# Optimization experiments

Hardware: AMD Instinct MI355X
Metric: run time of the kernel (lower is better)

## Reference

```python
import jax, jax.numpy as jnp
import numpy as np

TOP_K = 8
NUM_EXPERTS = 64
TEMPERATURE = 1.0
ALPHA = 0.01
EPS = 1e-20


def setup_inputs() -> dict:
    key = jax.random.key(0)
    k1, k2 = jax.random.split(key)
    hidden_states = jax.random.normal(k1, (4, 8192, 1024), dtype=jnp.float32)
    # kaiming_uniform-ish scale for the router weight
    bound = 1.0 / np.sqrt(1024.0)
    weight = jax.random.uniform(k2, (NUM_EXPERTS, 1024), dtype=jnp.float32,
                                minval=-bound, maxval=bound)
    return {"hidden_states": hidden_states, "weight": weight}


def reference(hidden_states, weight):
    bsz, seq_len, hidden_dim = hidden_states.shape
    flat = hidden_states.reshape(-1, hidden_dim)            # [N, H], N = bsz*seq_len
    logits = jnp.einsum('nh,eh->ne', flat, weight) / TEMPERATURE  # [N, E]
    scores = jax.nn.softmax(logits, axis=-1)                # [N, E]
    topk_weight, topk_idx = jax.lax.top_k(scores, TOP_K)    # [N, k] each
    # renormalize top-k probabilities
    topk_weight = topk_weight / (topk_weight.sum(axis=-1, keepdims=True) + EPS)
    # aux load-balancing loss (seq_aux=False branch), scores detached
    scores_aux = jax.lax.stop_gradient(scores)
    idx_flat = topk_idx.reshape(-1)                         # [N*k]
    ce = jnp.zeros((NUM_EXPERTS,), dtype=jnp.float32).at[idx_flat].add(1.0)
    ce = ce / idx_flat.shape[0]                             # mean of one-hot rows
    pi = scores_aux.mean(axis=0)                            # [E]
    fi = ce * NUM_EXPERTS
    aux_loss = (pi * fi).sum() * ALPHA
    return topk_idx, topk_weight, aux_loss
```

## Files before the change

### kernel.cpp

```cpp
#include <hip/hip_runtime.h>

#define H 1024
#define E 64
#define BT 64
#define THETA 1e-4f

typedef __attribute__((ext_vector_type(4))) float f4;
typedef __attribute__((ext_vector_type(2))) float f2;

__device__ __forceinline__ void pkfma(f2& acc, f2 a, f2 b) {
    asm("v_pk_fma_f32 %0, %1, %2, %0" : "+v"(acc) : "v"(a), "v"(b));
}

__device__ __forceinline__ void async16(const void* g, void* l) {
    __builtin_amdgcn_global_load_lds(
        (const __attribute__((address_space(1))) unsigned int*)g,
        (__attribute__((address_space(3))) unsigned int*)l,
        16, 0, 0);
}

__global__ __launch_bounds__(256, 2)
void gate_main(const float* __restrict__ hs, const float* __restrict__ wt,
               float* __restrict__ out, float* __restrict__ pi_ws,
               float* __restrict__ ce_ws, unsigned int* __restrict__ risk_cnt,
               unsigned int* __restrict__ risk_list, unsigned int risk_cap,
               int n_tokens) {
    __shared__ float smem[16384];
    const int t = threadIdx.x;
    const int wave = t >> 6, lane = t & 63;
    const int tok_base = blockIdx.x * BT;
    const int tg = t >> 4;
    const int eg = t & 15;

    f2 acc[4][4];
    #pragma unroll
    for (int j = 0; j < 4; ++j)
        #pragma unroll
        for (int i = 0; i < 4; ++i) acc[j][i] = (f2){0.f, 0.f};

    auto stage = [&](int c, int b) {
        const int bb = b * 8192;
        #pragma unroll
        for (int q = 0; q < 4; ++q) {
            const int L = q * 256 + t;
            const int row = L >> 4, j = L & 15;
            const int srcj = j ^ ((row >> 2) & 7);
            const float* gh = hs + (size_t)(tok_base + row) * H + c * 64 + srcj * 4;
            async16(gh, smem + bb + (q * 256 + wave * 64) * 4);
            const float* gw = wt + (size_t)row * H + c * 64 + srcj * 4;
            async16(gw, smem + bb + 4096 + (q * 256 + wave * 64) * 4);
        }
    };

    stage(0, 0);
    const int swh = tg & 7, swe = eg & 7;
    for (int c = 0; c < 16; ++c) {
        __syncthreads();
        if (c < 15) stage(c + 1, (c + 1) & 1);
        const f4* hb = (const f4*)(smem + (c & 1) * 8192);
        const f4* wb = hb + 1024;
        #pragma unroll
        for (int kq = 0; kq < 16; ++kq) {
            f4 hv[4], wv[4];
            #pragma unroll
            for (int j = 0; j < 4; ++j) hv[j] = hb[(tg * 4 + j) * 16 + (kq ^ swh)];
            #pragma unroll
            for (int i = 0; i < 4; ++i) wv[i] = wb[(eg * 4 + i) * 16 + (kq ^ swe)];
            #pragma unroll
            for (int j = 0; j < 4; ++j)
                #pragma unroll
                for (int i = 0; i < 4; ++i) {
                    pkfma(acc[j][i], __builtin_shufflevector(hv[j], hv[j], 0, 1),
                                     __builtin_shufflevector(wv[i], wv[i], 0, 1));
                    pkfma(acc[j][i], __builtin_shufflevector(hv[j], hv[j], 2, 3),
                                     __builtin_shufflevector(wv[i], wv[i], 2, 3));
                }
        }
    }
    __syncthreads();

    f4* S4 = (f4*)smem;
    float* S = smem;
    float* recip = smem + 4352;
    float* hist  = smem + 4416;
    float* pi3   = smem + 4480;
    #pragma unroll
    for (int j = 0; j < 4; ++j) {
        f4 v;
        v.x = acc[j][0].x + acc[j][0].y;
        v.y = acc[j][1].x + acc[j][1].y;
        v.z = acc[j][2].x + acc[j][2].y;
        v.w = acc[j][3].x + acc[j][3].y;
        S4[(tg * 4 + j) * 17 + eg] = v;
    }
    if (t < 64) hist[t] = 0.f;
    __syncthreads();

    {
        const int tok = t >> 2, q = t & 3;
        f4 v[4];
        #pragma unroll
        for (int c = 0; c < 4; ++c) v[c] = S4[tok * 17 + q * 4 + c];
        float m = v[0].x;
        #pragma unroll
        for (int c = 0; c < 4; ++c)
            m = fmaxf(m, fmaxf(fmaxf(v[c].x, v[c].y), fmaxf(v[c].z, v[c].w)));
        m = fmaxf(m, __shfl_xor(m, 1, 64));
        m = fmaxf(m, __shfl_xor(m, 2, 64));
        float lsum = 0.f;
        #pragma unroll
        for (int c = 0; c < 4; ++c) {
            v[c].x = __expf(v[c].x - m); v[c].y = __expf(v[c].y - m);
            v[c].z = __expf(v[c].z - m); v[c].w = __expf(v[c].w - m);
            lsum += (v[c].x + v[c].y) + (v[c].z + v[c].w);
        }
        #pragma unroll
        for (int c = 0; c < 4; ++c) S4[tok * 17 + q * 4 + c] = v[c];
        lsum += __shfl_xor(lsum, 1, 64);
        lsum += __shfl_xor(lsum, 2, 64);
        if (q == 0) recip[tok] = 1.0f / lsum;
    }
    __syncthreads();

    const int selw = blockIdx.x & 3;
    if (wave == selw) {
        const int tok = lane;
        const int tok_g = tok_base + tok;
        float val[9]; int idx[9];
        #pragma unroll
        for (int r = 0; r < 9; ++r) { val[r] = -1.f; idx[r] = 0; }
        #pragma unroll
        for (int c = 0; c < 16; ++c) {
            f4 v = S4[tok * 17 + c];
            float e4[4] = {v.x, v.y, v.z, v.w};
            #pragma unroll
            for (int u = 0; u < 4; ++u) {
                float cv = e4[u]; int ci = c * 4 + u;
                #pragma unroll
                for (int r = 0; r < 9; ++r) {
                    const bool g = cv > val[r];
                    const float tv = val[r]; const int ti = idx[r];
                    val[r] = g ? cv : tv;  idx[r] = g ? ci : ti;
                    cv = g ? tv : cv;      ci = g ? ti : ci;
                }
            }
        }
        const float s8 = ((val[0] + val[1]) + (val[2] + val[3]))
                       + ((val[4] + val[5]) + (val[6] + val[7]));
        const float wsum = s8 + 1e-20f;
        f4* out4 = (f4*)out;
        f4 o;
        o.x = (float)idx[0]; o.y = (float)idx[1]; o.z = (float)idx[2]; o.w = (float)idx[3];
        out4[(size_t)tok_g * 2] = o;
        o.x = (float)idx[4]; o.y = (float)idx[5]; o.z = (float)idx[6]; o.w = (float)idx[7];
        out4[(size_t)tok_g * 2 + 1] = o;
        const size_t wb = (size_t)n_tokens * 2;
        o.x = val[0] / wsum; o.y = val[1] / wsum; o.z = val[2] / wsum; o.w = val[3] / wsum;
        out4[wb + (size_t)tok_g * 2] = o;
        o.x = val[4] / wsum; o.y = val[5] / wsum; o.z = val[6] / wsum; o.w = val[7] / wsum;
        out4[wb + (size_t)tok_g * 2 + 1] = o;
        #pragma unroll
        for (int r = 0; r < 8; ++r) atomicAdd(&hist[idx[r]], 1.0f);
        float ming = 1e30f;
        #pragma unroll
        for (int r = 0; r < 8; ++r)
            ming = fminf(ming, (val[r] - val[r + 1]) / fmaxf(val[r], 1e-30f));
        if (ming < THETA) {
            unsigned int pos = atomicAdd(risk_cnt, 1u);
            if (pos < risk_cap) risk_list[pos] = (unsigned int)tok_g;
        }
    } else {
        const int third = ((wave - selw) & 3) - 1;
        const int e = lane;
        const int t0 = third * 21;
        const int t1 = (third == 2) ? 64 : (t0 + 21);
        float part = 0.f;
        for (int tok = t0; tok < t1; ++tok)
            part = fmaf(S[tok * 68 + e], recip[tok], part);
        pi3[third * 64 + e] = part;
    }
    __syncthreads();
    if (t < 64)       atomicAdd(&pi_ws[t], pi3[t] + pi3[64 + t] + pi3[128 + t]);
    else if (t < 128) atomicAdd(&ce_ws[t - 64], hist[t - 64]);
}

__global__ __launch_bounds__(256)
void gate_fixup(const float* __restrict__ hs, const float* __restrict__ wt,
                float* __restrict__ out, const unsigned int* __restrict__ risk_cnt,
                const unsigned int* __restrict__ risk_list, unsigned int risk_cap,
                int n_tokens) {
    __shared__ float hrow[H];
    __shared__ double red[256];
    unsigned int cnt = *risk_cnt;
    if (cnt > risk_cap) cnt = risk_cap;
    const int t = threadIdx.x;

    for (unsigned int u = blockIdx.x; u < cnt; u += gridDim.x) {
        const int tok = (int)risk_list[u];
        ((float4*)hrow)[t] = ((const float4*)(hs + (size_t)tok * H))[t];
        __syncthreads();

        const int e = t >> 2, sl = t & 3;
        const float4* wp = (const float4*)wt + (size_t)e * 256;
        const float4* hp = (const float4*)hrow;
        double acc = 0.0;
        #pragma unroll 8
        for (int k4 = 0; k4 < 64; ++k4) {
            float4 wv = wp[k4 * 4 + sl];
            float4 hv = hp[k4 * 4 + sl];
            acc = fma((double)wv.x, (double)hv.x, acc);
            acc = fma((double)wv.y, (double)hv.y, acc);
            acc = fma((double)wv.z, (double)hv.z, acc);
            acc = fma((double)wv.w, (double)hv.w, acc);
        }
        red[t] = acc;
        __syncthreads();

        if (t < 64) {
            const int lane = t;
            double lg = red[t * 4] + red[t * 4 + 1] + red[t * 4 + 2] + red[t * 4 + 3];
            double m = lg;
            #pragma unroll
            for (int off = 32; off > 0; off >>= 1) {
                double o = __shfl_xor(m, off, 64);
                m = (o > m) ? o : m;
            }
            const double p = exp(lg - m);
            double v = lg, psum = 0.0, mypv = 0.0;
            int myidx = 0;
            for (int r = 0; r < 8; ++r) {
                double bv = v; int bi = lane;
                #pragma unroll
                for (int off = 32; off > 0; off >>= 1) {
                    double ov = __shfl_xor(bv, off, 64);
                    int    oi = __shfl_xor(bi, off, 64);
                    if (ov > bv || (ov == bv && oi < bi)) { bv = ov; bi = oi; }
                }
                double pw = __shfl(p, bi, 64);
                psum += pw;
                if (lane == r) { myidx = bi; mypv = pw; }
                if (lane == bi) v = -1e300;
            }
            const double wsum = psum + 1e-20;
            if (lane < 8) {
                out[(size_t)tok * 8 + lane] = (float)myidx;
                out[(size_t)n_tokens * 8 + (size_t)tok * 8 + lane] = (float)(mypv / wsum);
            }
        }
        __syncthreads();
    }
}

__global__ void gate_aux(const float* __restrict__ pi_ws, const float* __restrict__ ce_ws,
                         float* __restrict__ out, int n_tokens) {
    const int lane = threadIdx.x;
    double pi = (double)pi_ws[lane] / (double)n_tokens;
    double ce = (double)ce_ws[lane] / ((double)n_tokens * 8.0);
    double term = pi * ce * 64.0;
    #pragma unroll
    for (int off = 32; off > 0; off >>= 1) term += __shfl_xor(term, off, 64);
    if (lane == 0) out[(size_t)n_tokens * 16] = (float)(term * 0.01);
}

extern "C" void kernel_launch(void* const* d_in, const int* in_sizes, int n_in,
                              void* d_out, int out_size, void* d_ws, size_t ws_size,
                              hipStream_t stream) {
    const float* hs = (const float*)d_in[0];
    const float* wt = (const float*)d_in[1];
    float* out = (float*)d_out;
    const int n_tokens = in_sizes[0] / H;

    float* pi_ws = (float*)d_ws;
    float* ce_ws = (float*)((char*)d_ws + 256);
    unsigned int* risk_cnt  = (unsigned int*)((char*)d_ws + 512);
    unsigned int* risk_list = (unsigned int*)((char*)d_ws + 1024);
    unsigned int risk_cap = (unsigned int)((ws_size > 1024 ? (ws_size - 1024) : 0) / 4);
    if (risk_cap > (unsigned int)n_tokens) risk_cap = (unsigned int)n_tokens;

    size_t zbytes = ws_size < 1024 ? ws_size : 1024;
    hipMemsetAsync(d_ws, 0, zbytes, stream);

    gate_main<<<n_tokens / BT, 256, 0, stream>>>(hs, wt, out, pi_ws, ce_ws,
                                                 risk_cnt, risk_list, risk_cap, n_tokens);
    gate_fixup<<<256, 256, 0, stream>>>(hs, wt, out, risk_cnt, risk_list, risk_cap, n_tokens);
    gate_aux<<<1, 64, 0, stream>>>(pi_ws, ce_ws, out, n_tokens);
}
```

Baseline: 244.9 us.

## Compute router logits with split-bf16 MFMA and fold aux kernel into fixup

Replaces the FP32 packed-FMA logits GEMM with bf16 MFMA 32x32x16 instructions. Each fp32 operand is split into hi and lo bf16 parts in registers and three MFMAs per step approximate fp32 accuracy. Staging moves from async global-to-LDS copies to register loads, conversion and LDS writes, with a new swizzled layout. The risk threshold is widened to catch the larger error near ties, which sends more tokens to the fixup path. The separate aux-loss kernel is merged into block 0 of the fixup kernel to save one launch.

```diff
diff --git a/kernel.cpp b/kernel.cpp
--- a/kernel.cpp
+++ b/kernel.cpp
@@ -3,20 +3,32 @@
 #define H 1024
 #define E 64
 #define BT 64
-#define THETA 1e-4f
+#define THETA 4e-4f
 
 typedef __attribute__((ext_vector_type(4))) float f4;
-typedef __attribute__((ext_vector_type(2))) float f2;
-
-__device__ __forceinline__ void pkfma(f2& acc, f2 a, f2 b) {
-    asm("v_pk_fma_f32 %0, %1, %2, %0" : "+v"(acc) : "v"(a), "v"(b));
-}
-
-__device__ __forceinline__ void async16(const void* g, void* l) {
-    __builtin_amdgcn_global_load_lds(
-        (const __attribute__((address_space(1))) unsigned int*)g,
-        (__attribute__((address_space(3))) unsigned int*)l,
-        16, 0, 0);
+typedef __attribute__((ext_vector_type(16))) float f32x16;
+typedef __bf16 bf16x8 __attribute__((ext_vector_type(8)));
+typedef unsigned int u32;
+typedef __attribute__((ext_vector_type(4))) u32 u32x4;
+
+__device__ __forceinline__ u32 cvtpk_bf16(float a, float b) {
+    u32 r;
+    asm("v_cvt_pk_bf16_f32 %0, %1, %2" : "=v"(r) : "v"(a), "v"(b));
+    return r;
+}
+__device__ __forceinline__ float asfloat(u32 u) { union { u32 u; float f; } c; c.u = u; return c.f; }
+
+__device__ __forceinline__ void split8(f4 a, f4 b, u32x4& hi, u32x4& lo) {
+    float x0[4] = {a.x, a.z, b.x, b.z};
+    float x1[4] = {a.y, a.w, b.y, b.w};
+    #pragma unroll
+    for (int i = 0; i < 4; ++i) {
+        u32 h = cvtpk_bf16(x0[i], x1[i]);
+        float r0 = x0[i] - asfloat(h << 16);
+        float r1 = x1[i] - asfloat(h & 0xFFFF0000u);
+        hi[i] = h;
+        lo[i] = cvtpk_bf16(r0, r1);
+    }
 }
 
 __global__ __launch_bounds__(256, 2)
@@ -29,69 +41,92 @@
     const int t = threadIdx.x;
     const int wave = t >> 6, lane = t & 63;
     const int tok_base = blockIdx.x * BT;
-    const int tg = t >> 4;
-    const int eg = t & 15;
-
-    f2 acc[4][4];
+
+    const int srow = t >> 3;
+    const int sjp  = t & 7;
+    const int ssw  = ((sjp ^ (srow & 7)) << 4);
+
+    const int lr   = lane & 31;
+    const int kh   = lane >> 5;
+    const int wrow = (wave >> 1) * 32;
+    const int wcol = (wave & 1) * 32;
+    const int aOff = (wrow + lr) * 128;
+    const int bOff = 16384 + (wcol + lr) * 128;
+    const int rsw  = lr & 7;
+
+    f32x16 acc0, acc1;
     #pragma unroll
-    for (int j = 0; j < 4; ++j)
-        #pragma unroll
-        for (int i = 0; i < 4; ++i) acc[j][i] = (f2){0.f, 0.f};
-
-    auto stage = [&](int c, int b) {
-        const int bb = b * 8192;
-        #pragma unroll
-        for (int q = 0; q < 4; ++q) {
-            const int L = q * 256 + t;
-            const int row = L >> 4, j = L & 15;
-            const int srcj = j ^ ((row >> 2) & 7);
-            const float* gh = hs + (size_t)(tok_base + row) * H + c * 64 + srcj * 4;
-            async16(gh, smem + bb + (q * 256 + wave * 64) * 4);
-            const float* gw = wt + (size_t)row * H + c * 64 + srcj * 4;
-            async16(gw, smem + bb + 4096 + (q * 256 + wave * 64) * 4);
-        }
+    for (int i = 0; i < 16; ++i) { acc0[i] = 0.f; acc1[i] = 0.f; }
+
+    f4 sreg[8];
+    char* sb = (char*)smem;
+
+    auto stage_load = [&](int c) {
+        const float* ph = hs + (size_t)(tok_base + srow) * H + c * 64 + sjp * 8;
+        sreg[0] = *(const f4*)ph;
+        sreg[1] = *(const f4*)(ph + 4);
+        sreg[2] = *(const f4*)(ph + 32 * H);
+        sreg[3] = *(const f4*)(ph + 32 * H + 4);
+        const float* pw = wt + (size_t)srow * H + c * 64 + sjp * 8;
+        sreg[4] = *(const f4*)pw;
+        sreg[5] = *(const f4*)(pw + 4);
+        sreg[6] = *(const f4*)(pw + 32 * H);
+        sreg[7] = *(const f4*)(pw + 32 * H + 4);
     };
-
-    stage(0, 0);
-    const int swh = tg & 7, swe = eg & 7;
+    auto stage_write = [&](int c) {
+        char* bb = sb + (c & 1) * 32768;
+        u32x4 hi, lo;
+        split8(sreg[0], sreg[1], hi, lo);
+        *(u32x4*)(bb + srow * 128 + ssw) = hi;
+        *(u32x4*)(bb + 8192 + srow * 128 + ssw) = lo;
+        split8(sreg[2], sreg[3], hi, lo);
+        *(u32x4*)(bb + (srow + 32) * 128 + ssw) = hi;
+        *(u32x4*)(bb + 8192 + (srow + 32) * 128 + ssw) = lo;
+        split8(sreg[4], sreg[5], hi, lo);
+        *(u32x4*)(bb + 16384 + srow * 128 + ssw) = hi;
+        *(u32x4*)(bb + 24576 + srow * 128 + ssw) = lo;
+        split8(sreg[6], sreg[7], hi, lo);
+        *(u32x4*)(bb + 16384 + (srow + 32) * 128 + ssw) = hi;
+        *(u32x4*)(bb + 24576 + (srow + 32) * 128 + ssw) = lo;
+    };
+
+    stage_load(0);
+    stage_write(0);
+    #pragma unroll 2
     for (int c = 0; c < 16; ++c) {
         __syncthreads();
-        if (c < 15) stage(c + 1, (c + 1) & 1);
-        const f4* hb = (const f4*)(smem + (c & 1) * 8192);
-        const f4* wb = hb + 1024;
-        #pragma unroll
-        for (int kq = 0; kq < 16; ++kq) {
-            f4 hv[4], wv[4];
-            #pragma unroll
-            for (int j = 0; j < 4; ++j) hv[j] = hb[(tg * 4 + j) * 16 + (kq ^ swh)];
-            #pragma unroll
-            for (int i = 0; i < 4; ++i) wv[i] = wb[(eg * 4 + i) * 16 + (kq ^ swe)];
-            #pragma unroll
-            for (int j = 0; j < 4; ++j)
-                #pragma unroll
-                for (int i = 0; i < 4; ++i) {
-                    pkfma(acc[j][i], __builtin_shufflevector(hv[j], hv[j], 0, 1),
-                                     __builtin_shufflevector(wv[i], wv[i], 0, 1));
-                    pkfma(acc[j][i], __builtin_shufflevector(hv[j], hv[j], 2, 3),
-                                     __builtin_shufflevector(wv[i], wv[i], 2, 3));
-                }
-        }
+        if (c < 15) stage_load(c + 1);
+        const char* cb = sb + (c & 1) * 32768;
+        #pragma unroll
+        for (int kk = 0; kk < 4; ++kk) {
+            const int g = ((kk * 2 + kh) ^ rsw) << 4;
+            bf16x8 ah = *(const bf16x8*)(cb + aOff + g);
+            bf16x8 al = *(const bf16x8*)(cb + 8192 + aOff + g);
+            bf16x8 bh = *(const bf16x8*)(cb + bOff + g);
+            bf16x8 bl = *(const bf16x8*)(cb + 8192 + bOff + g);
+            acc0 = __builtin_amdgcn_mfma_f32_32x32x16_bf16(ah, bh, acc0, 0, 0, 0);
+            acc1 = __builtin_amdgcn_mfma_f32_32x32x16_bf16(ah, bl, acc1, 0, 0, 0);
+            acc1 = __builtin_amdgcn_mfma_f32_32x32x16_bf16(al, bh, acc1, 0, 0, 0);
+        }
+        __builtin_amdgcn_sched_barrier(0);
+        if (c < 15) stage_write(c + 1);
     }
     __syncthreads();
 
+    float* S = smem;
     f4* S4 = (f4*)smem;
-    float* S = smem;
     float* recip = smem + 4352;
     float* hist  = smem + 4416;
     float* pi3   = smem + 4480;
-    #pragma unroll
-    for (int j = 0; j < 4; ++j) {
-        f4 v;
-        v.x = acc[j][0].x + acc[j][0].y;
-        v.y = acc[j][1].x + acc[j][1].y;
-        v.z = acc[j][2].x + acc[j][2].y;
-        v.w = acc[j][3].x + acc[j][3].y;
-        S4[(tg * 4 + j) * 17 + eg] = v;
+    {
+        const int col = wcol + lr;
+        #pragma unroll
+        for (int gq = 0; gq < 4; ++gq)
+            #pragma unroll
+            for (int q = 0; q < 4; ++q) {
+                const int row = wrow + gq * 8 + kh * 4 + q;
+                S[row * 68 + col] = acc0[gq * 4 + q] + acc1[gq * 4 + q];
+            }
     }
     if (t < 64) hist[t] = 0.f;
     __syncthreads();
@@ -100,22 +135,22 @@
         const int tok = t >> 2, q = t & 3;
         f4 v[4];
         #pragma unroll
-        for (int c = 0; c < 4; ++c) v[c] = S4[tok * 17 + q * 4 + c];
+        for (int c2 = 0; c2 < 4; ++c2) v[c2] = S4[tok * 17 + q * 4 + c2];
         float m = v[0].x;
         #pragma unroll
-        for (int c = 0; c < 4; ++c)
-            m = fmaxf(m, fmaxf(fmaxf(v[c].x, v[c].y), fmaxf(v[c].z, v[c].w)));
+        for (int c2 = 0; c2 < 4; ++c2)
+            m = fmaxf(m, fmaxf(fmaxf(v[c2].x, v[c2].y), fmaxf(v[c2].z, v[c2].w)));
         m = fmaxf(m, __shfl_xor(m, 1, 64));
         m = fmaxf(m, __shfl_xor(m, 2, 64));
         float lsum = 0.f;
         #pragma unroll
-        for (int c = 0; c < 4; ++c) {
-            v[c].x = __expf(v[c].x - m); v[c].y = __expf(v[c].y - m);
-            v[c].z = __expf(v[c].z - m); v[c].w = __expf(v[c].w - m);
-            lsum += (v[c].x + v[c].y) + (v[c].z + v[c].w);
-        }
-        #pragma unroll
-        for (int c = 0; c < 4; ++c) S4[tok * 17 + q * 4 + c] = v[c];
+        for (int c2 = 0; c2 < 4; ++c2) {
+            v[c2].x = __expf(v[c2].x - m); v[c2].y = __expf(v[c2].y - m);
+            v[c2].z = __expf(v[c2].z - m); v[c2].w = __expf(v[c2].w - m);
+            lsum += (v[c2].x + v[c2].y) + (v[c2].z + v[c2].w);
+        }
+        #pragma unroll
+        for (int c2 = 0; c2 < 4; ++c2) S4[tok * 17 + q * 4 + c2] = v[c2];
         lsum += __shfl_xor(lsum, 1, 64);
         lsum += __shfl_xor(lsum, 2, 64);
         if (q == 0) recip[tok] = 1.0f / lsum;
@@ -130,12 +165,12 @@
         #pragma unroll
         for (int r = 0; r < 9; ++r) { val[r] = -1.f; idx[r] = 0; }
         #pragma unroll
-        for (int c = 0; c < 16; ++c) {
-            f4 v = S4[tok * 17 + c];
+        for (int c2 = 0; c2 < 16; ++c2) {
+            f4 v = S4[tok * 17 + c2];
             float e4[4] = {v.x, v.y, v.z, v.w};
             #pragma unroll
             for (int u = 0; u < 4; ++u) {
-                float cv = e4[u]; int ci = c * 4 + u;
+                float cv = e4[u]; int ci = c2 * 4 + u;
                 #pragma unroll
                 for (int r = 0; r < 9; ++r) {
                     const bool g = cv > val[r];
@@ -188,12 +223,23 @@
 void gate_fixup(const float* __restrict__ hs, const float* __restrict__ wt,
                 float* __restrict__ out, const unsigned int* __restrict__ risk_cnt,
                 const unsigned int* __restrict__ risk_list, unsigned int risk_cap,
-                int n_tokens) {
+                int n_tokens, const float* __restrict__ pi_ws,
+                const float* __restrict__ ce_ws) {
     __shared__ float hrow[H];
     __shared__ double red[256];
+    const int t = threadIdx.x;
+
+    if (blockIdx.x == 0 && t < 64) {
+        double pi = (double)pi_ws[t] / (double)n_tokens;
+        double ce = (double)ce_ws[t] / ((double)n_tokens * 8.0);
+        double term = pi * ce * 64.0;
+        #pragma unroll
+        for (int off = 32; off > 0; off >>= 1) term += __shfl_xor(term, off, 64);
+        if (t == 0) out[(size_t)n_tokens * 16] = (float)(term * 0.01);
+    }
+
     unsigned int cnt = *risk_cnt;
     if (cnt > risk_cap) cnt = risk_cap;
-    const int t = threadIdx.x;
 
     for (unsigned int u = blockIdx.x; u < cnt; u += gridDim.x) {
         const int tok = (int)risk_list[u];
@@ -251,17 +297,6 @@
     }
 }
 
-__global__ void gate_aux(const float* __restrict__ pi_ws, const float* __restrict__ ce_ws,
-                         float* __restrict__ out, int n_tokens) {
-    const int lane = threadIdx.x;
-    double pi = (double)pi_ws[lane] / (double)n_tokens;
-    double ce = (double)ce_ws[lane] / ((double)n_tokens * 8.0);
-    double term = pi * ce * 64.0;
-    #pragma unroll
-    for (int off = 32; off > 0; off >>= 1) term += __shfl_xor(term, off, 64);
-    if (lane == 0) out[(size_t)n_tokens * 16] = (float)(term * 0.01);
-}
-
 extern "C" void kernel_launch(void* const* d_in, const int* in_sizes, int n_in,
                               void* d_out, int out_size, void* d_ws, size_t ws_size,
                               hipStream_t stream) {
@@ -282,6 +317,6 @@
 
     gate_main<<<n_tokens / BT, 256, 0, stream>>>(hs, wt, out, pi_ws, ce_ws,
                                                  risk_cnt, risk_list, risk_cap, n_tokens);
-    gate_fixup<<<256, 256, 0, stream>>>(hs, wt, out, risk_cnt, risk_list, risk_cap, n_tokens);
-    gate_aux<<<1, 64, 0, stream>>>(pi_ws, ce_ws, out, n_tokens);
-}
+    gate_fixup<<<256, 256, 0, stream>>>(hs, wt, out, risk_cnt, risk_list, risk_cap,
+                                        n_tokens, pi_ws, ce_ws);
+}
```

Result: slower. 274.7 us (+12.2%).
